# Kernel optimization log

Measured on AMD Instinct MI355X. Metric: run time of the kernel, lower is better.

## Reference

```python
import jax, jax.numpy as jnp
import numpy as np
from math import sqrt

NUM_HEADS = 16
NUM_KV_HEADS = 4
ROPE_BASE = 10000.0


def setup_inputs() -> dict:
    key = jax.random.key(0)
    ks = jax.random.split(key, 9)
    B, S, E = 4, 2048, 2048
    KV_DIM = NUM_KV_HEADS * (E // NUM_HEADS)  # 512
    s = 0.02
    return {
        "x": jax.random.normal(ks[0], (B, S, E), jnp.float32),
        "wq": jax.random.normal(ks[1], (E, E), jnp.float32) * s,
        "bq": jnp.zeros((E,), jnp.float32),
        "wk": jax.random.normal(ks[2], (KV_DIM, E), jnp.float32) * s,
        "bk": jnp.zeros((KV_DIM,), jnp.float32),
        "wv": jax.random.normal(ks[3], (KV_DIM, E), jnp.float32) * s,
        "bv": jnp.zeros((KV_DIM,), jnp.float32),
        "wo": jax.random.normal(ks[4], (E, E), jnp.float32) * s,
        "bo": jnp.zeros((E,), jnp.float32),
    }


def _rope_cos_sin(seq_len, head_dim, dtype):
    inv_freq = 1.0 / (ROPE_BASE ** (jnp.arange(0, head_dim, 2, dtype=jnp.float32) / head_dim))
    pos = jnp.arange(seq_len, dtype=jnp.float32)
    freqs = pos[:, None] * inv_freq[None, :]            # [S, D/2]
    emb = jnp.concatenate([freqs, freqs], axis=-1)      # [S, D]
    return jnp.cos(emb).astype(dtype), jnp.sin(emb).astype(dtype)


def _apply_rope(t, cos, sin):
    # t: [B, H, S, D]; cos/sin: [S, D]
    d2 = t.shape[-1] // 2
    rot = jnp.concatenate([-t[..., d2:], t[..., :d2]], axis=-1)
    return t * cos[None, None, :, :] + rot * sin[None, None, :, :]


def reference(x, wq, bq, wk, bk, wv, bv, wo, bo):
    B, S, E = x.shape
    H, KV = NUM_HEADS, NUM_KV_HEADS
    D = E // H
    G = H // KV

    q = (x @ wq.T + bq).reshape(B, S, H, D).transpose(0, 2, 1, 3)   # [B,H,S,D]
    k = (x @ wk.T + bk).reshape(B, S, KV, D).transpose(0, 2, 1, 3)  # [B,KV,S,D]
    v = (x @ wv.T + bv).reshape(B, S, KV, D).transpose(0, 2, 1, 3)

    cos, sin = _rope_cos_sin(S, D, x.dtype)
    q = _apply_rope(q, cos, sin)
    k = _apply_rope(k, cos, sin)

    # GQA: expand each kv head group_size times (contiguous repeat)
    k = jnp.repeat(k, G, axis=1)  # [B,H,S,D]
    v = jnp.repeat(v, G, axis=1)

    scores = jnp.einsum("bhqd,bhkd->bhqk", q, k)
    causal = jnp.triu(jnp.ones((S, S), dtype=bool), k=1)
    scores = jnp.where(causal[None, None, :, :], -jnp.inf, scores)
    attn = jax.nn.softmax(scores / sqrt(D), axis=-1)
    out = jnp.einsum("bhqk,bhkd->bhqd", attn, v)        # [B,H,S,D]
    out = out.transpose(0, 2, 1, 3).reshape(B, S, E)
    return out @ wo.T + bo
```

## Files before the change

### kernel.cpp

```cpp
#include <hip/hip_runtime.h>
#include <stdint.h>
#include <math.h>

typedef __attribute__((ext_vector_type(8))) short s16x8;
typedef __attribute__((ext_vector_type(4))) short s16x4;
typedef __attribute__((ext_vector_type(4))) float f32x4;

#define NEGH (-1.0e30f)

__device__ __forceinline__ short f2bf(float f) {
  union { float f; unsigned int i; } c; c.f = f;
  unsigned int lsb = (c.i >> 16) & 1u;
  c.i += 0x7fffu + lsb;
  return (short)(c.i >> 16);
}
__device__ __forceinline__ float bf2f(short u) {
  union { unsigned int i; float f; } c;
  c.i = ((unsigned int)(unsigned short)u) << 16;
  return c.f;
}

#define GLOAD_LDS16(gp, lp)                                                  \
  __builtin_amdgcn_global_load_lds(                                          \
      (__attribute__((address_space(1))) void*)(void*)(gp),                  \
      (__attribute__((address_space(3))) void*)(lp), 16, 0, 0)

__global__ __launch_bounds__(256) void cvt_kernel(const float* __restrict__ in,
                                                  short* __restrict__ out)
{
  const size_t i = ((size_t)blockIdx.x * 256 + threadIdx.x) * 4;
  const float4 v = *(const float4*)(in + i);
  s16x4 o = { f2bf(v.x), f2bf(v.y), f2bf(v.z), f2bf(v.w) };
  *(s16x4*)(out + i) = o;
}

__global__ __launch_bounds__(256) void wcvt_kernel(
    const float* __restrict__ wq, const float* __restrict__ wk,
    const float* __restrict__ wv, short* __restrict__ wqb,
    short* __restrict__ wkb, short* __restrict__ wvb,
    float2* __restrict__ tab)
{
  const int bid = blockIdx.x;
  if (bid < 6144) {
    const float* in; short* out; int lb;
    if (bid < 4096)      { in = wq; out = wqb; lb = bid; }
    else if (bid < 5120) { in = wk; out = wkb; lb = bid - 4096; }
    else                 { in = wv; out = wvb; lb = bid - 5120; }
    const size_t i = ((size_t)lb * 256 + threadIdx.x) * 4;
    const float4 v = *(const float4*)(in + i);
    s16x4 o = { f2bf(v.x), f2bf(v.y), f2bf(v.z), f2bf(v.w) };
    *(s16x4*)(out + i) = o;
  } else {
    const int i = (bid - 6144) * 256 + threadIdx.x;
    const int d = i & 63;
    const float fr = (float)(i >> 6) * exp2f((float)d * -0.20762050593048584f);
    float sn, cs;
    sincosf(fr, &sn, &cs);
    tab[i] = make_float2(cs, sn);
  }
}

__global__ __launch_bounds__(256) void gemm_bt(
    const short* __restrict__ A, const short* __restrict__ W,
    const float* __restrict__ bias, const float* __restrict__ bias2,
    void* __restrict__ C, void* __restrict__ C2,
    int M, int N, int K, int omode)
{
  __shared__ __align__(16) short As[128 * 64];
  __shared__ __align__(16) short Bs[128 * 64];

  const int t = threadIdx.x;
  const int l = t & 63;
  const int w = t >> 6;
  const int lane16 = l & 15;
  const int quad = l >> 4;
  const int wm = w >> 1, wn = w & 1;

  int bx = blockIdx.x, by = blockIdx.y;
  if (gridDim.x == 8 && gridDim.y == 64) {
    const int lid = blockIdx.x + 8 * blockIdx.y;
    const int xcd = lid & 7, idx = lid >> 3;
    by = xcd * 8 + (idx >> 3);
    bx = idx & 7;
  }
  const int mb0 = by * 128;
  const int nb0 = bx * 128;

  const f32x4 zero = {0.f, 0.f, 0.f, 0.f};
  f32x4 acc[4][4];
#pragma unroll
  for (int i = 0; i < 4; ++i)
#pragma unroll
    for (int j = 0; j < 4; ++j) acc[i][j] = zero;

  const int sr = t >> 3;
  const int sp = t & 7;
  const short* Ag = A + (size_t)(mb0 + sr) * K + sp * 8;
  const short* Wg = W + (size_t)(nb0 + sr) * K + sp * 8;
  short* Al = As + t * 8;
  short* Bl = Bs + t * 8;

  const int nkt = K >> 6;
  for (int kt = 0; kt < nkt; ++kt) {
    __syncthreads();
    const int kof = kt * 64;
#pragma unroll
    for (int it = 0; it < 4; ++it) {
      GLOAD_LDS16(Ag + kof + (size_t)(it * 32) * K, Al + it * 2048);
      GLOAD_LDS16(Wg + kof + (size_t)(it * 32) * K, Bl + it * 2048);
    }
    __syncthreads();
#pragma unroll
    for (int kk = 0; kk < 2; ++kk) {
      s16x8 af[4], bf[4];
#pragma unroll
      for (int mi = 0; mi < 4; ++mi)
        af[mi] = *(const s16x8*)&As[(wm * 64 + mi * 16 + lane16) * 64 +
                                    kk * 32 + quad * 8];
#pragma unroll
      for (int ni = 0; ni < 4; ++ni)
        bf[ni] = *(const s16x8*)&Bs[(wn * 64 + ni * 16 + lane16) * 64 +
                                    kk * 32 + quad * 8];
#pragma unroll
      for (int mi = 0; mi < 4; ++mi)
#pragma unroll
        for (int ni = 0; ni < 4; ++ni)
          acc[mi][ni] = __builtin_amdgcn_mfma_f32_16x16x32_bf16(
              af[mi], bf[ni], acc[mi][ni], 0, 0, 0);
    }
  }

#pragma unroll
  for (int ni = 0; ni < 4; ++ni) {
    const int n = nb0 + wn * 64 + ni * 16 + lane16;
    const float bvx = (omode == 3 && n >= 512) ? bias2[n - 512] : bias[n];
#pragma unroll
    for (int mi = 0; mi < 4; ++mi) {
      const int m0 = mb0 + wm * 64 + mi * 16 + quad * 4;
#pragma unroll
      for (int r = 0; r < 4; ++r) {
        const int m = m0 + r;
        const float v = acc[mi][ni][r] + bvx;
        if (omode == 0) {
          ((short*)C)[(size_t)m * N + n] = f2bf(v);
        } else if (omode == 1) {
          ((float*)C)[(size_t)m * N + n] = v;
        } else {
          if (n < 512) ((short*)C)[(size_t)m * 512 + n] = f2bf(v);
          else         ((short*)C2)[(size_t)m * 512 + (n - 512)] = f2bf(v);
        }
      }
    }
  }
}

__global__ __launch_bounds__(512, 2) void gemm256_bt(
    const short* __restrict__ A, const short* __restrict__ W,
    const float* __restrict__ bias, void* __restrict__ C,
    int M, int N, int K, int omode)
{
  __shared__ __align__(16) short Asm[2 * 16384];
  __shared__ __align__(16) short Bsm[2 * 16384];

  const int t = threadIdx.x;
  const int l = t & 63;
  const int w = t >> 6;
  const int lane16 = l & 15;
  const int quad = l >> 4;
  const int wm = w >> 2;
  const int wn = w & 3;

  int bx = blockIdx.x, by = blockIdx.y;
  if (gridDim.x == 8 && gridDim.y == 32) {
    const int bid = blockIdx.y * 8 + blockIdx.x;
    const int xcd = bid & 7, idx = bid >> 3;
    const int xc = xcd & 3, yc = xcd >> 2;
    bx = xc * 2 + (idx & 1);
    by = yc * 16 + (idx >> 1);
  }
  const int mb0 = by * 256;
  const int nb0 = bx * 256;

  const f32x4 zero = {0.f, 0.f, 0.f, 0.f};
  f32x4 acc[8][4];
#pragma unroll
  for (int i = 0; i < 8; ++i)
#pragma unroll
    for (int j = 0; j < 4; ++j) acc[i][j] = zero;

  const int srow = t >> 2;
  const int scs = (t & 3) ^ ((t >> 3) & 3);
  const short* Ag = A + (size_t)(mb0 + srow) * K + scs * 8;
  const short* Wg = W + (size_t)(nb0 + srow) * K + scs * 8;
  const size_t rstep = (size_t)128 * K;

#define STAGE_A(b, kt, kh)                                                    \
  do {                                                                        \
    const size_t ko_ = (size_t)(kt) * 64 + (kh) * 32;                         \
    GLOAD_LDS16(Ag + ko_,         Asm + (b) * 16384 + (kh) * 8192 + t * 8);   \
    GLOAD_LDS16(Ag + ko_ + rstep, Asm + (b) * 16384 + (kh) * 8192 + 4096 + t * 8); \
  } while (0)
#define STAGE_B(b, kt, kh)                                                    \
  do {                                                                        \
    const size_t ko_ = (size_t)(kt) * 64 + (kh) * 32;                         \
    GLOAD_LDS16(Wg + ko_,         Bsm + (b) * 16384 + (kh) * 8192 + t * 8);   \
    GLOAD_LDS16(Wg + ko_ + rstep, Bsm + (b) * 16384 + (kh) * 8192 + 4096 + t * 8); \
  } while (0)

#define VMW6                                                                  \
  asm volatile("s_waitcnt vmcnt(6)" ::: "memory");                            \
  __builtin_amdgcn_sched_barrier(0);

  s16x8 bfr[4];

#define DO_PHASE(BUF, KK, MG, READB, STAGE_STMT, VM_STMT)                     \
  {                                                                           \
    const short* Abase = Asm + (BUF) * 16384 + (KK) * 8192;                   \
    const short* Bbase = Bsm + (BUF) * 16384 + (KK) * 8192;                   \
    if (READB) {                                                              \
      _Pragma("unroll")                                                       \
      for (int ni = 0; ni < 4; ++ni) {                                        \
        const int nr = wn * 64 + ni * 16 + lane16;                            \
        bfr[ni] = *(const s16x8*)(Bbase + nr * 32 +                           \
                                  ((quad ^ ((nr >> 1) & 3)) << 3));           \
      }                                                                       \
    }                                                                         \
    s16x8 afr[4];                                                             \
    _Pragma("unroll")                                                         \
    for (int mi2 = 0; mi2 < 4; ++mi2) {                                       \
      const int mr = wm * 128 + (MG) * 64 + mi2 * 16 + lane16;                \
      afr[mi2] = *(const s16x8*)(Abase + mr * 32 +                            \
                                 ((quad ^ ((mr >> 1) & 3)) << 3));            \
    }                                                                         \
    STAGE_STMT;                                                               \
    __builtin_amdgcn_s_barrier();                                             \
    asm volatile("s_waitcnt lgkmcnt(0)" ::: "memory");                        \
    __builtin_amdgcn_sched_barrier(0);                                        \
    __builtin_amdgcn_s_setprio(1);                                            \
    _Pragma("unroll")                                                         \
    for (int mi2 = 0; mi2 < 4; ++mi2)                                         \
      _Pragma("unroll")                                                       \
      for (int ni = 0; ni < 4; ++ni)                                          \
        acc[(MG) * 4 + mi2][ni] = __builtin_amdgcn_mfma_f32_16x16x32_bf16(    \
            afr[mi2], bfr[ni], acc[(MG) * 4 + mi2][ni], 0, 0, 0);             \
    __builtin_amdgcn_s_setprio(0);                                            \
    VM_STMT                                                                   \
    __builtin_amdgcn_s_barrier();                                             \
  }

  const int NT = K >> 6;

  STAGE_B(0, 0, 0); STAGE_A(0, 0, 0); STAGE_B(0, 0, 1); STAGE_A(0, 0, 1);
  STAGE_B(1, 1, 0); STAGE_A(1, 1, 0); STAGE_B(1, 1, 1);
  asm volatile("s_waitcnt vmcnt(6)" ::: "memory");
  __builtin_amdgcn_sched_barrier(0);
  __builtin_amdgcn_s_barrier();

  for (int i2 = 0; i2 < NT; i2 += 2) {
    const int tp1 = (i2 + 1 < NT) ? i2 + 1 : NT - 1;
    const int tp2 = (i2 + 2 < NT) ? i2 + 2 : NT - 1;
    const int tp3 = (i2 + 3 < NT) ? i2 + 3 : NT - 1;
    DO_PHASE(0, 0, 0, true,  STAGE_A(1, tp1, 1), )
    DO_PHASE(0, 0, 1, false, STAGE_B(0, tp2, 0), )
    DO_PHASE(0, 1, 0, true,  STAGE_A(0, tp2, 0), )
    DO_PHASE(0, 1, 1, false, STAGE_B(0, tp2, 1), VMW6)
    DO_PHASE(1, 0, 0, true,  STAGE_A(0, tp2, 1), )
    DO_PHASE(1, 0, 1, false, STAGE_B(1, tp3, 0), )
    DO_PHASE(1, 1, 0, true,  STAGE_A(1, tp3, 0), )
    DO_PHASE(1, 1, 1, false, STAGE_B(1, tp3, 1), VMW6)
  }

#pragma unroll
  for (int ni = 0; ni < 4; ++ni) {
    const int n = nb0 + wn * 64 + ni * 16 + lane16;
    const float bv = bias[n];
#pragma unroll
    for (int mi = 0; mi < 8; ++mi) {
      const int m0 = mb0 + wm * 128 + mi * 16 + quad * 4;
#pragma unroll
      for (int r = 0; r < 4; ++r) {
        const float v = acc[mi][ni][r] + bv;
        if (omode == 0) ((short*)C)[(size_t)(m0 + r) * N + n] = f2bf(v);
        else            ((float*)C)[(size_t)(m0 + r) * N + n] = v;
      }
    }
  }
#undef DO_PHASE
#undef STAGE_A
#undef STAGE_B
#undef VMW6
}

__global__ __launch_bounds__(256) void rope_kernel(short* __restrict__ buf,
                                                   int lognh,
                                                   const float2* __restrict__ tab)
{
  const int idx = blockIdx.x * 256 + threadIdx.x;
  const int d = idx & 63;
  const int rest = idx >> 6;
  const int row = rest >> lognh;
  const int pos = row & 2047;
  const float2 cssn = tab[(pos << 6) | d];
  const float cs = cssn.x, sn = cssn.y;
  const size_t base = (size_t)rest * 128 + d;
  const float lo = bf2f(buf[base]);
  const float hi = bf2f(buf[base + 64]);
  buf[base]      = f2bf(lo * cs - hi * sn);
  buf[base + 64] = f2bf(hi * cs + lo * sn);
}

__global__ __launch_bounds__(256) void trans_kernel(const short* __restrict__ in,
                                                    short* __restrict__ out)
{
  __shared__ short T[64 * 72];
  const int t = threadIdx.x;
  const int ms = blockIdx.x * 64;
  const int ns = blockIdx.y * 64;
  const int b = ms >> 11;
  const int sl = ms & 2047;
  const int r = t >> 3, sg = t & 7;
#pragma unroll
  for (int j = 0; j < 2; ++j) {
    const uint4 v = *(const uint4*)(in + (size_t)(ms + r + 32 * j) * 512 + ns + sg * 8);
    *(uint4*)&T[(r + 32 * j) * 72 + sg * 8] = v;
  }
  __syncthreads();
#pragma unroll
  for (int j = 0; j < 2; ++j) {
    const int nr = r + 32 * j;
    s16x8 v;
#pragma unroll
    for (int i = 0; i < 8; ++i) v[i] = T[(sg * 8 + i) * 72 + nr];
    *(s16x8*)(out + ((size_t)(b * 512 + ns + nr)) * 2048 + sl + sg * 8) = v;
  }
}

__global__ __launch_bounds__(512, 4) void attn_kernel(
    const short* __restrict__ qg, const short* __restrict__ kg,
    const short* __restrict__ vtg, short* __restrict__ og,
    const float2* __restrict__ tab)
{
  __shared__ __align__(16) short Ksm[2 * 64 * 128];
  __shared__ __align__(16) short Vsm[2 * 128 * 64];
  __shared__ __align__(16) short Psm[128 * 64];

  const int t = threadIdx.x;
  const int l = t & 63;
  const int w = t >> 6;
  const int lane16 = l & 15;
  const int quad = l >> 4;

  const int lid = blockIdx.x + 8 * (blockIdx.y + 16 * blockIdx.z);
  const int xcd = lid & 7, idx = lid >> 3;
  const int g = xcd * 2 + (idx >> 5);
  const int wv_ = idx & 31;
  const int b = g >> 2, kv = g & 3;
  const int h = kv * 4 + (wv_ >> 3);
  const int jb = wv_ & 7;

  const int krow = t >> 4, kseg = t & 15;
  const int vrow = t >> 3, vseg = t & 7;
  const int kswz = (kseg ^ (krow & 7)) * 8;
  const int vswz = (vseg ^ (vrow & 7)) * 8;

  const short* kbaseptr = kg + ((size_t)(b * 2048)) * 512 + kv * 128;
  const short* vbaseptr = vtg + ((size_t)(b * 512 + kv * 128)) * 2048;

  const float SC = 0.08838834764831845f * 1.4426950408889634f;
  const f32x4 zero = {0.f, 0.f, 0.f, 0.f};
  const int swz = (lane16 & 7) << 3;

  uint4 kr0, kr1, vr0, vr1;
#define LOADT()                                                               \
  do {                                                                        \
    kr0 = *(const uint4*)kld;                                                 \
    kr1 = *(const uint4*)(kld + 32 * 512);                                    \
    vr0 = *(const uint4*)vld;                                                 \
    vr1 = *(const uint4*)(vld + 64 * 2048);                                   \
    kld += 64 * 512;                                                          \
    vld += 64;                                                                \
  } while (0)
#define WRITET(c)                                                             \
  do {                                                                        \
    *(uint4*)&Ksm[(c) * 8192 + krow * 128 + kswz] = kr0;                      \
    *(uint4*)&Ksm[(c) * 8192 + (32 + krow) * 128 + kswz] = kr1;               \
    *(uint4*)&Vsm[(c) * 8192 + vrow * 64 + vswz] = vr0;                       \
    *(uint4*)&Vsm[(c) * 8192 + (64 + vrow) * 64 + vswz] = vr1;                \
  } while (0)

  for (int sp2 = 0; sp2 < 2; ++sp2) {
    const int jj = sp2 ? (15 - jb) : jb;
    const int qb0 = jj * 128;
    const int qw0 = qb0 + w * 16;
    const int qmaxw = qw0 + 15;
    const int ntl = 2 * jj + 2;

    const short* kld = kbaseptr + (size_t)krow * 512 + kseg * 8;
    const short* vld = vbaseptr + (size_t)vrow * 2048 + vseg * 8;

    s16x8 qf[4];
    {
      const short* qrow =
          qg + ((size_t)(b * 2048 + qw0 + lane16)) * 2048 + h * 128 + quad * 8;
      s16x8 qr[4];
#pragma unroll
      for (int kk = 0; kk < 4; ++kk) qr[kk] = *(const s16x8*)(qrow + kk * 32);
      const float2* tb = tab + (((size_t)(qw0 + lane16)) << 6) + quad * 8;
#pragma unroll
      for (int kk = 0; kk < 2; ++kk) {
        float lo[8], hi[8];
#pragma unroll
        for (int j = 0; j < 8; ++j) {
          const float2 cs2 = tb[kk * 32 + j];
          const float l0 = bf2f(qr[kk][j]);
          const float h0 = bf2f(qr[kk + 2][j]);
          lo[j] = l0 * cs2.x - h0 * cs2.y;
          hi[j] = h0 * cs2.x + l0 * cs2.y;
        }
        union { unsigned int u[4]; s16x8 v; } plo, phi;
#pragma unroll
        for (int j = 0; j < 4; ++j) {
          asm("v_cvt_pk_bf16_f32 %0, %1, %2"
              : "=v"(plo.u[j]) : "v"(lo[2 * j]), "v"(lo[2 * j + 1]));
          asm("v_cvt_pk_bf16_f32 %0, %1, %2"
              : "=v"(phi.u[j]) : "v"(hi[2 * j]), "v"(hi[2 * j + 1]));
        }
        qf[kk] = plo.v;
        qf[kk + 2] = phi.v;
      }
    }

    f32x4 o[8];
#pragma unroll
    for (int i = 0; i < 8; ++i) o[i] = zero;
    float m_i = NEGH, l_i = 0.f;

    LOADT();
    WRITET(0);
    __syncthreads();
    int cur = 0;

    for (int tl = 0; tl < ntl; ++tl) {
      const int kbase = tl * 64;
      if (tl + 1 < ntl) LOADT();

      if (kbase <= qmaxw) {
        const short* Kb = Ksm + cur * 8192;
        const short* Vb = Vsm + cur * 8192;
        f32x4 st[4];
#pragma unroll
        for (int mt = 0; mt < 4; ++mt) st[mt] = zero;
        __builtin_amdgcn_s_setprio(1);
#pragma unroll
        for (int mt = 0; mt < 4; ++mt) {
          const int rb = (mt * 16 + lane16) * 128;
#pragma unroll
          for (int kk = 0; kk < 4; ++kk) {
            const s16x8 a = *(const s16x8*)&Kb[rb + ((kk * 32 + quad * 8) ^ swz)];
            st[mt] = __builtin_amdgcn_mfma_f32_16x16x32_bf16(a, qf[kk], st[mt], 0, 0, 0);
          }
        }
        __builtin_amdgcn_s_setprio(0);

        const bool maskt = (kbase + 63 > qw0);
        const int qabs = qw0 + lane16;
        if (maskt) {
#pragma unroll
          for (int mt = 0; mt < 4; ++mt)
#pragma unroll
            for (int r = 0; r < 4; ++r) {
              if ((kbase + mt * 16 + quad * 4 + r) > qabs) st[mt][r] = NEGH;
            }
        }
        float tm[4];
#pragma unroll
        for (int mt = 0; mt < 4; ++mt)
          tm[mt] = fmaxf(fmaxf(st[mt][0], st[mt][1]),
                         fmaxf(st[mt][2], st[mt][3]));
        float tl_ = fmaxf(fmaxf(tm[0], tm[1]), fmaxf(tm[2], tm[3]));
        tl_ = fmaxf(tl_, __shfl_xor(tl_, 16));
        tl_ = fmaxf(tl_, __shfl_xor(tl_, 32));
        const float mnew = fmaxf(m_i, tl_);
        if (!__all(tl_ <= m_i)) {
          const float alpha = exp2f((m_i - mnew) * SC);
          l_i *= alpha;
#pragma unroll
          for (int r = 0; r < 4; ++r) {
            const float ar = __shfl(alpha, quad * 4 + r);
#pragma unroll
            for (int ntd = 0; ntd < 8; ++ntd) o[ntd][r] *= ar;
          }
        }
        m_i = mnew;
        const float mS = mnew * SC;
        float rs = 0.f;
#pragma unroll
        for (int mt = 0; mt < 4; ++mt) {
          const float p0 = exp2f(fmaf(st[mt][0], SC, -mS));
          const float p1 = exp2f(fmaf(st[mt][1], SC, -mS));
          const float p2 = exp2f(fmaf(st[mt][2], SC, -mS));
          const float p3 = exp2f(fmaf(st[mt][3], SC, -mS));
          rs += (p0 + p1) + (p2 + p3);
          uint2 pk2;
          asm("v_cvt_pk_bf16_f32 %0, %1, %2" : "=v"(pk2.x) : "v"(p0), "v"(p1));
          asm("v_cvt_pk_bf16_f32 %0, %1, %2" : "=v"(pk2.y) : "v"(p2), "v"(p3));
          *(uint2*)&Psm[(w * 16 + lane16) * 64 + ((mt * 16 + quad * 4) ^ swz)] = pk2;
        }
        rs += __shfl_xor(rs, 16);
        rs += __shfl_xor(rs, 32);
        l_i += rs;

        const int prb = (w * 16 + lane16) * 64;
        __builtin_amdgcn_s_setprio(1);
#pragma unroll
        for (int kk = 0; kk < 2; ++kk) {
          const s16x8 pf = *(const s16x8*)&Psm[prb + ((kk * 32 + quad * 8) ^ swz)];
#pragma unroll
          for (int ntd = 0; ntd < 8; ++ntd) {
            const s16x8 vf =
                *(const s16x8*)&Vb[(ntd * 16 + lane16) * 64 + ((kk * 32 + quad * 8) ^ swz)];
            o[ntd] = __builtin_amdgcn_mfma_f32_16x16x32_bf16(pf, vf, o[ntd], 0, 0, 0);
          }
        }
        __builtin_amdgcn_s_setprio(0);
      }

      if (tl + 1 < ntl) WRITET(cur ^ 1);
      __syncthreads();
      cur ^= 1;
    }

#pragma unroll
    for (int r = 0; r < 4; ++r) {
      const float lr = __shfl(l_i, quad * 4 + r);
      const float inv = 1.f / lr;
      const size_t base =
          ((size_t)(b * 2048 + qw0 + quad * 4 + r)) * 2048 + h * 128 + lane16;
#pragma unroll
      for (int ntd = 0; ntd < 8; ++ntd) og[base + ntd * 16] = f2bf(o[ntd][r] * inv);
    }
  }
#undef LOADT
#undef WRITET
}

extern "C" void kernel_launch(void* const* d_in, const int* in_sizes, int n_in,
                              void* d_out, int out_size, void* d_ws,
                              size_t ws_size, hipStream_t stream)
{
  const float* x  = (const float*)d_in[0];
  const float* wq = (const float*)d_in[1];
  const float* bq = (const float*)d_in[2];
  const float* wk = (const float*)d_in[3];
  const float* bk = (const float*)d_in[4];
  const float* wv = (const float*)d_in[5];
  const float* bv = (const float*)d_in[6];
  const float* wo = (const float*)d_in[7];
  const float* bo = (const float*)d_in[8];
  float* out = (float*)d_out;

  char* ws = (char*)d_ws;
  short* xb  = (short*)ws;
  short* wqb = (short*)(ws + (32ull << 20));
  short* wkb = (short*)(ws + (40ull << 20));
  short* wvb = (short*)(ws + (42ull << 20));
  short* qws = (short*)(ws + (44ull << 20));
  float2* tab = (float2*)(ws + (76ull << 20));
  short* wob = xb;
  short* kws = (short*)d_out;
  short* vtw = (short*)((char*)d_out + (8ull << 20));
  short* vtmp = (short*)((char*)d_out + (16ull << 20));

  const dim3 blk(256);
  cvt_kernel<<<16384, blk, 0, stream>>>(x, xb);
  wcvt_kernel<<<6656, blk, 0, stream>>>(wq, wkb == 0 ? 0 : wk, wv, wqb, wkb, wvb, tab);
  gemm256_bt<<<dim3(8, 32), dim3(512), 0, stream>>>(xb, wqb, bq, qws, 8192, 2048, 2048, 0);
  gemm_bt<<<dim3(8, 64), blk, 0, stream>>>(xb, wkb, bk, bv, kws, vtmp, 8192, 1024, 2048, 3);
  trans_kernel<<<dim3(128, 8), blk, 0, stream>>>(vtmp, vtw);
  rope_kernel<<<8192, blk, 0, stream>>>(kws, 2, tab);
  cvt_kernel<<<4096, blk, 0, stream>>>(wo, wob);
  attn_kernel<<<dim3(8, 16, 4), dim3(512), 0, stream>>>(qws, kws, vtw, qws, tab);
  gemm256_bt<<<dim3(8, 32), dim3(512), 0, stream>>>(qws, wob, bo, out, 8192, 2048, 2048, 1);
}
```

Measured before the change: 492.8 us.

## Give each attention wave two 16-row query strips with half the waves

The attention block drops from 8 to 4 waves, and each wave now handles 32 query rows as two 16-row strips. Each K fragment read from LDS now feeds two MFMAs, and each V fragment feeds two PV MFMAs, so LDS traffic per FLOP is halved. The tile loading is spread over fewer threads, so each thread loads four vectors instead of two. The cost is roughly double the accumulator registers per wave and fewer waves per block to hide latency. Launch bounds change to (256, 2).

```diff
diff --git a/kernel.cpp b/kernel.cpp
--- a/kernel.cpp
+++ b/kernel.cpp
@@ -335,7 +335,7 @@
   }
 }
 
-__global__ __launch_bounds__(512, 4) void attn_kernel(
+__global__ __launch_bounds__(256, 2) void attn_kernel(
     const short* __restrict__ qg, const short* __restrict__ kg,
     const short* __restrict__ vtg, short* __restrict__ og,
     const float2* __restrict__ tab)
@@ -370,42 +370,51 @@
   const f32x4 zero = {0.f, 0.f, 0.f, 0.f};
   const int swz = (lane16 & 7) << 3;
 
-  uint4 kr0, kr1, vr0, vr1;
+  uint4 kr[4], vr[4];
 #define LOADT()                                                               \
   do {                                                                        \
-    kr0 = *(const uint4*)kld;                                                 \
-    kr1 = *(const uint4*)(kld + 32 * 512);                                    \
-    vr0 = *(const uint4*)vld;                                                 \
-    vr1 = *(const uint4*)(vld + 64 * 2048);                                   \
+    kr[0] = *(const uint4*)kld;                                               \
+    kr[1] = *(const uint4*)(kld + 16 * 512);                                  \
+    kr[2] = *(const uint4*)(kld + 32 * 512);                                  \
+    kr[3] = *(const uint4*)(kld + 48 * 512);                                  \
+    vr[0] = *(const uint4*)vld;                                               \
+    vr[1] = *(const uint4*)(vld + 32 * 2048);                                 \
+    vr[2] = *(const uint4*)(vld + 64 * 2048);                                 \
+    vr[3] = *(const uint4*)(vld + 96 * 2048);                                 \
     kld += 64 * 512;                                                          \
     vld += 64;                                                                \
   } while (0)
 #define WRITET(c)                                                             \
   do {                                                                        \
-    *(uint4*)&Ksm[(c) * 8192 + krow * 128 + kswz] = kr0;                      \
-    *(uint4*)&Ksm[(c) * 8192 + (32 + krow) * 128 + kswz] = kr1;               \
-    *(uint4*)&Vsm[(c) * 8192 + vrow * 64 + vswz] = vr0;                       \
-    *(uint4*)&Vsm[(c) * 8192 + (64 + vrow) * 64 + vswz] = vr1;                \
+    *(uint4*)&Ksm[(c) * 8192 + krow * 128 + kswz] = kr[0];                    \
+    *(uint4*)&Ksm[(c) * 8192 + (16 + krow) * 128 + kswz] = kr[1];             \
+    *(uint4*)&Ksm[(c) * 8192 + (32 + krow) * 128 + kswz] = kr[2];             \
+    *(uint4*)&Ksm[(c) * 8192 + (48 + krow) * 128 + kswz] = kr[3];             \
+    *(uint4*)&Vsm[(c) * 8192 + vrow * 64 + vswz] = vr[0];                     \
+    *(uint4*)&Vsm[(c) * 8192 + (32 + vrow) * 64 + vswz] = vr[1];              \
+    *(uint4*)&Vsm[(c) * 8192 + (64 + vrow) * 64 + vswz] = vr[2];              \
+    *(uint4*)&Vsm[(c) * 8192 + (96 + vrow) * 64 + vswz] = vr[3];              \
   } while (0)
 
   for (int sp2 = 0; sp2 < 2; ++sp2) {
     const int jj = sp2 ? (15 - jb) : jb;
     const int qb0 = jj * 128;
-    const int qw0 = qb0 + w * 16;
-    const int qmaxw = qw0 + 15;
+    const int qw0 = qb0 + w * 32;
+    const int qmaxw = qw0 + 31;
     const int ntl = 2 * jj + 2;
 
     const short* kld = kbaseptr + (size_t)krow * 512 + kseg * 8;
     const short* vld = vbaseptr + (size_t)vrow * 2048 + vseg * 8;
 
-    s16x8 qf[4];
-    {
+    s16x8 qf[2][4];
+#pragma unroll
+    for (int s = 0; s < 2; ++s) {
       const short* qrow =
-          qg + ((size_t)(b * 2048 + qw0 + lane16)) * 2048 + h * 128 + quad * 8;
+          qg + ((size_t)(b * 2048 + qw0 + s * 16 + lane16)) * 2048 + h * 128 + quad * 8;
       s16x8 qr[4];
 #pragma unroll
       for (int kk = 0; kk < 4; ++kk) qr[kk] = *(const s16x8*)(qrow + kk * 32);
-      const float2* tb = tab + (((size_t)(qw0 + lane16)) << 6) + quad * 8;
+      const float2* tb = tab + (((size_t)(qw0 + s * 16 + lane16)) << 6) + quad * 8;
 #pragma unroll
       for (int kk = 0; kk < 2; ++kk) {
         float lo[8], hi[8];
@@ -425,15 +434,18 @@
           asm("v_cvt_pk_bf16_f32 %0, %1, %2"
               : "=v"(phi.u[j]) : "v"(hi[2 * j]), "v"(hi[2 * j + 1]));
         }
-        qf[kk] = plo.v;
-        qf[kk + 2] = phi.v;
+        qf[s][kk] = plo.v;
+        qf[s][kk + 2] = phi.v;
       }
     }
 
-    f32x4 o[8];
-#pragma unroll
-    for (int i = 0; i < 8; ++i) o[i] = zero;
-    float m_i = NEGH, l_i = 0.f;
+    f32x4 o[2][8];
+#pragma unroll
+    for (int s = 0; s < 2; ++s)
+#pragma unroll
+      for (int i = 0; i < 8; ++i) o[s][i] = zero;
+    float m_i[2] = {NEGH, NEGH};
+    float l_i[2] = {0.f, 0.f};
 
     LOADT();
     WRITET(0);
@@ -447,9 +459,11 @@
       if (kbase <= qmaxw) {
         const short* Kb = Ksm + cur * 8192;
         const short* Vb = Vsm + cur * 8192;
-        f32x4 st[4];
-#pragma unroll
-        for (int mt = 0; mt < 4; ++mt) st[mt] = zero;
+        f32x4 st[2][4];
+#pragma unroll
+        for (int s = 0; s < 2; ++s)
+#pragma unroll
+          for (int mt = 0; mt < 4; ++mt) st[s][mt] = zero;
         __builtin_amdgcn_s_setprio(1);
 #pragma unroll
         for (int mt = 0; mt < 4; ++mt) {
@@ -457,69 +471,77 @@
 #pragma unroll
           for (int kk = 0; kk < 4; ++kk) {
             const s16x8 a = *(const s16x8*)&Kb[rb + ((kk * 32 + quad * 8) ^ swz)];
-            st[mt] = __builtin_amdgcn_mfma_f32_16x16x32_bf16(a, qf[kk], st[mt], 0, 0, 0);
+            st[0][mt] = __builtin_amdgcn_mfma_f32_16x16x32_bf16(a, qf[0][kk], st[0][mt], 0, 0, 0);
+            st[1][mt] = __builtin_amdgcn_mfma_f32_16x16x32_bf16(a, qf[1][kk], st[1][mt], 0, 0, 0);
           }
         }
         __builtin_amdgcn_s_setprio(0);
 
         const bool maskt = (kbase + 63 > qw0);
-        const int qabs = qw0 + lane16;
-        if (maskt) {
+#pragma unroll
+        for (int s = 0; s < 2; ++s) {
+          const int qabs = qw0 + s * 16 + lane16;
+          if (maskt) {
+#pragma unroll
+            for (int mt = 0; mt < 4; ++mt)
+#pragma unroll
+              for (int r = 0; r < 4; ++r) {
+                if ((kbase + mt * 16 + quad * 4 + r) > qabs) st[s][mt][r] = NEGH;
+              }
+          }
+          float tm[4];
 #pragma unroll
           for (int mt = 0; mt < 4; ++mt)
+            tm[mt] = fmaxf(fmaxf(st[s][mt][0], st[s][mt][1]),
+                           fmaxf(st[s][mt][2], st[s][mt][3]));
+          float tl_ = fmaxf(fmaxf(tm[0], tm[1]), fmaxf(tm[2], tm[3]));
+          tl_ = fmaxf(tl_, __shfl_xor(tl_, 16));
+          tl_ = fmaxf(tl_, __shfl_xor(tl_, 32));
+          const float mnew = fmaxf(m_i[s], tl_);
+          if (!__all(tl_ <= m_i[s])) {
+            const float alpha = exp2f((m_i[s] - mnew) * SC);
+            l_i[s] *= alpha;
 #pragma unroll
             for (int r = 0; r < 4; ++r) {
-              if ((kbase + mt * 16 + quad * 4 + r) > qabs) st[mt][r] = NEGH;
+              const float ar = __shfl(alpha, quad * 4 + r);
+#pragma unroll
+              for (int ntd = 0; ntd < 8; ++ntd) o[s][ntd][r] *= ar;
             }
+          }
+          m_i[s] = mnew;
+          const float mS = mnew * SC;
+          float rs = 0.f;
+#pragma unroll
+          for (int mt = 0; mt < 4; ++mt) {
+            const float p0 = exp2f(fmaf(st[s][mt][0], SC, -mS));
+            const float p1 = exp2f(fmaf(st[s][mt][1], SC, -mS));
+            const float p2 = exp2f(fmaf(st[s][mt][2], SC, -mS));
+            const float p3 = exp2f(fmaf(st[s][mt][3], SC, -mS));
+            rs += (p0 + p1) + (p2 + p3);
+            uint2 pk2;
+            asm("v_cvt_pk_bf16_f32 %0, %1, %2" : "=v"(pk2.x) : "v"(p0), "v"(p1));
+            asm("v_cvt_pk_bf16_f32 %0, %1, %2" : "=v"(pk2.y) : "v"(p2), "v"(p3));
+            *(uint2*)&Psm[(w * 32 + s * 16 + lane16) * 64 +
+                          ((mt * 16 + quad * 4) ^ swz)] = pk2;
+          }
+          rs += __shfl_xor(rs, 16);
+          rs += __shfl_xor(rs, 32);
+          l_i[s] += rs;
         }
-        float tm[4];
-#pragma unroll
-        for (int mt = 0; mt < 4; ++mt)
-          tm[mt] = fmaxf(fmaxf(st[mt][0], st[mt][1]),
-                         fmaxf(st[mt][2], st[mt][3]));
-        float tl_ = fmaxf(fmaxf(tm[0], tm[1]), fmaxf(tm[2], tm[3]));
-        tl_ = fmaxf(tl_, __shfl_xor(tl_, 16));
-        tl_ = fmaxf(tl_, __shfl_xor(tl_, 32));
-        const float mnew = fmaxf(m_i, tl_);
-        if (!__all(tl_ <= m_i)) {
-          const float alpha = exp2f((m_i - mnew) * SC);
-          l_i *= alpha;
-#pragma unroll
-          for (int r = 0; r < 4; ++r) {
-            const float ar = __shfl(alpha, quad * 4 + r);
-#pragma unroll
-            for (int ntd = 0; ntd < 8; ++ntd) o[ntd][r] *= ar;
-          }
-        }
-        m_i = mnew;
-        const float mS = mnew * SC;
-        float rs = 0.f;
-#pragma unroll
-        for (int mt = 0; mt < 4; ++mt) {
-          const float p0 = exp2f(fmaf(st[mt][0], SC, -mS));
-          const float p1 = exp2f(fmaf(st[mt][1], SC, -mS));
-          const float p2 = exp2f(fmaf(st[mt][2], SC, -mS));
-          const float p3 = exp2f(fmaf(st[mt][3], SC, -mS));
-          rs += (p0 + p1) + (p2 + p3);
-          uint2 pk2;
-          asm("v_cvt_pk_bf16_f32 %0, %1, %2" : "=v"(pk2.x) : "v"(p0), "v"(p1));
-          asm("v_cvt_pk_bf16_f32 %0, %1, %2" : "=v"(pk2.y) : "v"(p2), "v"(p3));
-          *(uint2*)&Psm[(w * 16 + lane16) * 64 + ((mt * 16 + quad * 4) ^ swz)] = pk2;
-        }
-        rs += __shfl_xor(rs, 16);
-        rs += __shfl_xor(rs, 32);
-        l_i += rs;
-
-        const int prb = (w * 16 + lane16) * 64;
+
+        const int prb0 = (w * 32 + lane16) * 64;
+        const int prb1 = (w * 32 + 16 + lane16) * 64;
         __builtin_amdgcn_s_setprio(1);
 #pragma unroll
         for (int kk = 0; kk < 2; ++kk) {
-          const s16x8 pf = *(const s16x8*)&Psm[prb + ((kk * 32 + quad * 8) ^ swz)];
+          const s16x8 pf0 = *(const s16x8*)&Psm[prb0 + ((kk * 32 + quad * 8) ^ swz)];
+          const s16x8 pf1 = *(const s16x8*)&Psm[prb1 + ((kk * 32 + quad * 8) ^ swz)];
 #pragma unroll
           for (int ntd = 0; ntd < 8; ++ntd) {
             const s16x8 vf =
                 *(const s16x8*)&Vb[(ntd * 16 + lane16) * 64 + ((kk * 32 + quad * 8) ^ swz)];
-            o[ntd] = __builtin_amdgcn_mfma_f32_16x16x32_bf16(pf, vf, o[ntd], 0, 0, 0);
+            o[0][ntd] = __builtin_amdgcn_mfma_f32_16x16x32_bf16(pf0, vf, o[0][ntd], 0, 0, 0);
+            o[1][ntd] = __builtin_amdgcn_mfma_f32_16x16x32_bf16(pf1, vf, o[1][ntd], 0, 0, 0);
           }
         }
         __builtin_amdgcn_s_setprio(0);
@@ -531,14 +553,18 @@
     }
 
 #pragma unroll
-    for (int r = 0; r < 4; ++r) {
-      const float lr = __shfl(l_i, quad * 4 + r);
-      const float inv = 1.f / lr;
-      const size_t base =
-          ((size_t)(b * 2048 + qw0 + quad * 4 + r)) * 2048 + h * 128 + lane16;
-#pragma unroll
-      for (int ntd = 0; ntd < 8; ++ntd) og[base + ntd * 16] = f2bf(o[ntd][r] * inv);
-    }
+    for (int s = 0; s < 2; ++s)
+#pragma unroll
+      for (int r = 0; r < 4; ++r) {
+        const float lr = __shfl(l_i[s], quad * 4 + r);
+        const float inv = 1.f / lr;
+        const size_t base =
+            ((size_t)(b * 2048 + qw0 + s * 16 + quad * 4 + r)) * 2048 +
+            h * 128 + lane16;
+#pragma unroll
+        for (int ntd = 0; ntd < 8; ++ntd)
+          og[base + ntd * 16] = f2bf(o[s][ntd][r] * inv);
+      }
   }
 #undef LOADT
 #undef WRITET
@@ -573,12 +599,12 @@
 
   const dim3 blk(256);
   cvt_kernel<<<16384, blk, 0, stream>>>(x, xb);
-  wcvt_kernel<<<6656, blk, 0, stream>>>(wq, wkb == 0 ? 0 : wk, wv, wqb, wkb, wvb, tab);
+  wcvt_kernel<<<6656, blk, 0, stream>>>(wq, wk, wv, wqb, wkb, wvb, tab);
   gemm256_bt<<<dim3(8, 32), dim3(512), 0, stream>>>(xb, wqb, bq, qws, 8192, 2048, 2048, 0);
   gemm_bt<<<dim3(8, 64), blk, 0, stream>>>(xb, wkb, bk, bv, kws, vtmp, 8192, 1024, 2048, 3);
   trans_kernel<<<dim3(128, 8), blk, 0, stream>>>(vtmp, vtw);
   rope_kernel<<<8192, blk, 0, stream>>>(kws, 2, tab);
   cvt_kernel<<<4096, blk, 0, stream>>>(wo, wob);
-  attn_kernel<<<dim3(8, 16, 4), dim3(512), 0, stream>>>(qws, kws, vtw, qws, tab);
+  attn_kernel<<<dim3(8, 16, 4), blk, 0, stream>>>(qws, kws, vtw, qws, tab);
   gemm256_bt<<<dim3(8, 32), dim3(512), 0, stream>>>(qws, wob, bo, out, 8192, 2048, 2048, 1);
 }
```

New measurement: 599.4 us. +21.6%, slower.
